# Kernel optimization log

Hardware: AMD Instinct MI355X
Metric: run time of the kernel (lower is better)

The kernel has to match this reference:

```python
import jax, jax.numpy as jnp
import numpy as np
from jax import lax

NUM_MELS = 80
NQ = 256          # num_quants
WIN = 1024
HOP = 256
K_UP = 800        # upsample kernel
PAD_UP = K_UP + 4 * HOP - WIN   # = 800
RC = 120          # residual_channels
SC = 240          # skip_channels
KC = 2            # causal kernel
NB = 16           # num blocks
DILS = [1, 2, 4, 8, 16, 32, 64, 128] * 2
DN = ('NCH', 'OIH', 'NCH')


def conv1x1(x, w, b):
    # x: [B,C,T], w: [O,C], b: [O]
    return jnp.einsum('bct,oc->bot', x, w) + b[None, :, None]


def causal_conv(x, w, b, d):
    # x: [B,RC,T], w: [2RC,RC,KC], left-pad by d*(KC-1) -> causal, same length
    y = lax.conv_general_dilated(x, w, (1,), [(d * (KC - 1), 0)],
                                 rhs_dilation=(d,), dimension_numbers=DN)
    return y + b[None, :, None]


def setup_inputs() -> dict:
    key = jax.random.key(0)
    ks = jax.random.split(key, 20)
    s = 0.05
    n = jax.random.normal
    return {
        'waveforms': n(ks[0], (1, 40960), jnp.float32),
        'melspecs': n(ks[1], (1, NUM_MELS, 160), jnp.float32),
        # ConvTranspose-equivalent upsample weight, stored as direct conv weight [O,I,K]
        'up_w': s * n(ks[2], (NUM_MELS, NUM_MELS, K_UP), jnp.float32),
        'up_b': jnp.zeros((NUM_MELS,), jnp.float32),
        'in_w': s * n(ks[3], (RC, 1), jnp.float32),
        'in_b': jnp.zeros((RC,), jnp.float32),
        'blk_causal_w': s * n(ks[4], (NB, 2 * RC, RC, KC), jnp.float32),
        'blk_causal_b': jnp.zeros((NB, 2 * RC), jnp.float32),
        'blk_cond_w': s * n(ks[5], (NB, 2 * RC, NUM_MELS), jnp.float32),
        'blk_cond_b': jnp.zeros((NB, 2 * RC), jnp.float32),
        'blk_skip_w': s * n(ks[6], (NB, SC, RC), jnp.float32),
        'blk_skip_b': jnp.zeros((NB, SC), jnp.float32),
        'blk_res_w': s * n(ks[7], (NB, RC, RC), jnp.float32),
        'blk_res_b': jnp.zeros((NB, RC), jnp.float32),
        'h1_w': s * n(ks[8], (NQ, SC), jnp.float32),
        'h1_b': jnp.zeros((NQ,), jnp.float32),
        'h2_w': s * n(ks[9], (NQ, NQ), jnp.float32),
        'h2_b': jnp.zeros((NQ,), jnp.float32),
    }


def _forward(waveforms, melspecs, up_w, up_b, in_w, in_b,
             blk_causal_w, blk_causal_b, blk_cond_w, blk_cond_b,
             blk_skip_w, blk_skip_b, blk_res_w, blk_res_b,
             h1_w, h1_b, h2_w, h2_b):
    # ConvTranspose1d(stride=HOP, padding=PAD_UP) as lhs-dilated conv:
    # out_len = (F-1)*HOP + K_UP - 2*PAD_UP
    cond = lax.conv_general_dilated(
        melspecs, up_w, (1,), [(K_UP - 1 - PAD_UP, K_UP - 1 - PAD_UP)],
        lhs_dilation=(HOP,), dimension_numbers=DN) + up_b[None, :, None]
    L = min(waveforms.shape[-1], cond.shape[-1])
    wav = waveforms[..., :L]
    cond = cond[..., :L]

    res = conv1x1(wav[:, None, :], in_w, in_b)          # [B,RC,L]
    skip_sum = jnp.zeros((res.shape[0], SC, L), res.dtype)
    for i, d in enumerate(DILS):
        z = causal_conv(res, blk_causal_w[i], blk_causal_b[i], d) \
            + conv1x1(cond, blk_cond_w[i], blk_cond_b[i])  # [B,2RC,L]
        h = jnp.tanh(z[:, :RC]) * jax.nn.sigmoid(z[:, RC:])
        skip_sum = skip_sum + conv1x1(h, blk_skip_w[i], blk_skip_b[i])
        res = res + conv1x1(h, blk_res_w[i], blk_res_b[i])

    x = jax.nn.relu(skip_sum)
    x = jax.nn.relu(conv1x1(x, h1_w, h1_b))
    logits = conv1x1(x, h2_w, h2_b)                      # [B,NQ,L]
    return logits


def reference(waveforms, melspecs, up_w, up_b, in_w, in_b,
              blk_causal_w, blk_causal_b, blk_cond_w, blk_cond_b,
              blk_skip_w, blk_skip_b, blk_res_w, blk_res_b,
              h1_w, h1_b, h2_w, h2_b):
    return _forward(waveforms, melspecs, up_w, up_b, in_w, in_b,
                    blk_causal_w, blk_causal_b, blk_cond_w, blk_cond_b,
                    blk_skip_w, blk_skip_b, blk_res_w, blk_res_b,
                    h1_w, h1_b, h2_w, h2_b)
```

## Files before the change

kernel.cpp:

```cpp
#include <hip/hip_runtime.h>

#define L_LEN 39904
#define NT 624
#define RCH 120
#define SCH 240
#define CMEL 80
#define NQO 256
#define NBLK 16
#define KUP 800

typedef unsigned short u16;
typedef __attribute__((ext_vector_type(8))) short short8;
typedef __attribute__((ext_vector_type(4))) float f32x4;

#define MFMA(a, b, c) __builtin_amdgcn_mfma_f32_16x16x32_bf16((a), (b), (c), 0, 0, 0)

__device__ __forceinline__ u16 f2bf(float f) {
    unsigned u = __float_as_uint(f);
    u += 0x7FFFu + ((u >> 16) & 1u);
    return (u16)(u >> 16);
}
__device__ __forceinline__ unsigned pack2(float a, float b) {
    return (unsigned)f2bf(a) | ((unsigned)f2bf(b) << 16);
}
__device__ __forceinline__ float b16tof(u16 h) {
    return __uint_as_float((unsigned)h << 16);
}
__device__ __forceinline__ float gate(float a, float b) {
    float ea = __expf(2.f * a);
    float th = 1.f - 2.f * __builtin_amdgcn_rcpf(ea + 1.f);
    float sg = __builtin_amdgcn_rcpf(1.f + __expf(-b));
    return th * sg;
}

constexpr size_t O_CONDT = 0;
constexpr size_t O_RESA  = O_CONDT + 7023104;
constexpr size_t O_RESB  = O_RESA + 19153920;
constexpr size_t O_SKIP  = O_RESB + 19153920;
constexpr size_t O_ZFRAG = O_SKIP + 19153920;
constexpr size_t O_SKF   = O_ZFRAG + 2621440;
constexpr size_t O_RF    = O_SKF + 1048576;
constexpr size_t O_H1F   = O_RF + 524288;
constexpr size_t O_H2F   = O_H1F + 131072;
constexpr size_t O_UPF   = O_H2F + 131072;
constexpr size_t O_ZB    = O_UPF + 13107200;
constexpr size_t O_SKB   = O_ZB + 16384;

constexpr size_t HO_RESA  = 7023104;
constexpr size_t HO_RESB  = HO_RESA + 19153920;
constexpr size_t HO_ZFRAG = HO_RESB + 19153920;
constexpr size_t HO_SKF   = HO_ZFRAG + 2621440;
constexpr size_t HO_RF    = HO_SKF + 1048576;
constexpr size_t HO_H1F   = HO_RF + 524288;
constexpr size_t HO_H2F   = HO_H1F + 131072;
constexpr size_t HO_ZB    = HO_H2F + 131072;
constexpr size_t HO_SKBS  = HO_ZB + 16384;
constexpr size_t HO_HALL  = HO_SKBS + 16384;
constexpr size_t H_BYTES  = (size_t)NBLK * L_LEN * 120 * 2;
constexpr size_t UPF_BYTES = 13107200;
constexpr size_t NEED_H = HO_HALL + (H_BYTES > UPF_BYTES ? H_BYTES : UPF_BYTES);

__global__ void k_prep_zfrag(const float* __restrict__ bc_w, const float* __restrict__ bq_w,
                             u16* __restrict__ dst) {
    int i = blockIdx.x * 256 + threadIdx.x;
    if (i >= NBLK * 10 * 16 * 512) return;
    int jj = i & 7, lane = (i >> 3) & 63, mt = (i >> 9) & 15;
    int rest = i >> 13, ks = rest % 10, blk = rest / 10;
    int m = mt * 16 + (lane & 15);
    int k = ks * 32 + ((lane >> 4) << 3) + jj;
    float v = 0.f;
    if (m < 240) {
        int o = (m & 1) ? (m >> 1) + 120 : (m >> 1);
        if (k < 120)       v = bc_w[((size_t)(blk * 240 + o) * 120 + k) * 2 + 0];
        else if (k < 240)  v = bc_w[((size_t)(blk * 240 + o) * 120 + (k - 120)) * 2 + 1];
        else               v = bq_w[(size_t)(blk * 240 + o) * 80 + (k - 240)];
    }
    dst[i] = f2bf(v);
}
__global__ void k_prep_skfrag(const float* __restrict__ bs_w, u16* __restrict__ dst) {
    int i = blockIdx.x * 256 + threadIdx.x;
    if (i >= NBLK * 4 * 16 * 512) return;
    int jj = i & 7, lane = (i >> 3) & 63, mt = (i >> 9) & 15;
    int rest = i >> 13, ks = rest & 3, blk = rest >> 2;
    int m = mt * 16 + (lane & 15);
    int k = ks * 32 + ((lane >> 4) << 3) + jj;
    float v = (m < 240 && k < 120) ? bs_w[(size_t)(blk * 240 + m) * 120 + k] : 0.f;
    dst[i] = f2bf(v);
}
__global__ void k_prep_rfrag(const float* __restrict__ br_w, u16* __restrict__ dst) {
    int i = blockIdx.x * 256 + threadIdx.x;
    if (i >= NBLK * 4 * 8 * 512) return;
    int jj = i & 7, lane = (i >> 3) & 63, mt = (i >> 9) & 7;
    int rest = i >> 12, ks = rest & 3, blk = rest >> 2;
    int m = mt * 16 + (lane & 15);
    int k = ks * 32 + ((lane >> 4) << 3) + jj;
    float v = (m < 120 && k < 120) ? br_w[(size_t)(blk * 120 + m) * 120 + k] : 0.f;
    dst[i] = f2bf(v);
}
__global__ void k_prep_h1frag(const float* __restrict__ h1_w, u16* __restrict__ dst) {
    int i = blockIdx.x * 256 + threadIdx.x;
    if (i >= 8 * 16 * 512) return;
    int jj = i & 7, lane = (i >> 3) & 63, mt = (i >> 9) & 15, ks = i >> 13;
    int m = mt * 16 + (lane & 15);
    int k = ks * 32 + ((lane >> 4) << 3) + jj;
    float v = (k < 240) ? h1_w[(size_t)m * 240 + k] : 0.f;
    dst[i] = f2bf(v);
}
__global__ void k_prep_h2frag(const float* __restrict__ h2_w, u16* __restrict__ dst) {
    int i = blockIdx.x * 256 + threadIdx.x;
    if (i >= 8 * 16 * 512) return;
    int jj = i & 7, lane = (i >> 3) & 63, mt = (i >> 9) & 15, ks = i >> 13;
    int m = mt * 16 + (lane & 15);
    int k = ks * 32 + ((lane >> 4) << 3) + jj;
    dst[i] = f2bf(h2_w[(size_t)m * 256 + k]);
}
__global__ void k_prep_upfrag(const float* __restrict__ up_w, u16* __restrict__ dst) {
    int i = blockIdx.x * 256 + threadIdx.x;
    if (i >= 256 * 10 * 5 * 512) return;
    int jj = i & 7, lane = (i >> 3) & 63;
    int rest = i >> 9;
    int mt = rest % 5; rest /= 5;
    int ks = rest % 10; int p = rest / 10;
    int m = mt * 16 + (lane & 15);
    int k = ks * 32 + ((lane >> 4) << 3) + jj;
    int c = k >> 2, j = k & 3;
    int r = (256 - ((p + 1) & 255)) & 255;
    int kk = r + 256 * j;
    float v = (m < 80 && kk < KUP) ? up_w[((size_t)m * 80 + c) * KUP + kk] : 0.f;
    dst[i] = f2bf(v);
}
__global__ void k_prep_zbias(const float* __restrict__ bc_b, const float* __restrict__ bq_b,
                             float* __restrict__ dst) {
    int i = blockIdx.x * 256 + threadIdx.x;
    if (i >= NBLK * 256) return;
    int m = i & 255, blk = i >> 8;
    float v = 0.f;
    if (m < 240) {
        int o = (m & 1) ? (m >> 1) + 120 : (m >> 1);
        v = bc_b[blk * 240 + o] + bq_b[blk * 240 + o];
    }
    dst[i] = v;
}
__global__ void k_prep_skbias(const float* __restrict__ bs_b, float* __restrict__ dst) {
    int i = blockIdx.x * 256 + threadIdx.x;
    if (i >= NBLK * 240) return;
    dst[i] = bs_b[i];
}
__global__ void k_prep_skbsum(const float* __restrict__ bs_b, float* __restrict__ dst) {
    int m = blockIdx.x * 256 + threadIdx.x;
    if (m >= 240) return;
    float s = 0.f;
    for (int i = 0; i < NBLK; i++) s += bs_b[i * 240 + m];
    dst[m] = s;
}
__global__ void k_res_initT(const float* __restrict__ wav, const float* __restrict__ in_w,
                            const float* __restrict__ in_b, float* __restrict__ resT) {
    int i = blockIdx.x * 256 + threadIdx.x;
    if (i >= L_LEN * RCH) return;
    int t = i / RCH, c = i % RCH;
    resT[i] = wav[t] * in_w[c] + in_b[c];
}

__global__ __launch_bounds__(256) void k_up(const float* __restrict__ mel,
        const u16* __restrict__ upf, const float* __restrict__ up_b,
        u16* __restrict__ condT) {
    __shared__ u16 s_ms[64 * 328];
    const int tid = threadIdx.x, l = tid & 63, w = tid >> 6;
    const int quad = l >> 4, tloc = l & 15;
    const int p = blockIdx.x, s0 = blockIdx.y * 64;
    for (int rr = 0; rr < 16; rr++) {
        int tt = w + 4 * rr;
        int sg = s0 + tt;
        #pragma unroll
        for (int base = 0; base < 320; base += 64) {
            int ck = base + l;
            int c = ck >> 2, j = ck & 3;
            int mi = 1 + j + sg;
            float v = (mi < 160) ? mel[c * 160 + mi] : 0.f;
            s_ms[tt * 328 + ck] = f2bf(v);
        }
    }
    __syncthreads();
    f32x4 acc[2][4];
    #pragma unroll
    for (int i = 0; i < 2; i++)
        #pragma unroll
        for (int n = 0; n < 4; n++) acc[i][n] = (f32x4){0.f, 0.f, 0.f, 0.f};
    const int nmt = (w == 0) ? 2 : 1;
    int mts[2]; mts[0] = w; mts[1] = 4;
    for (int ks = 0; ks < 10; ks++) {
        short8 b[4];
        int k0 = ks * 32 + quad * 8;
        #pragma unroll
        for (int n = 0; n < 4; n++)
            b[n] = *(const short8*)&s_ms[(n * 16 + tloc) * 328 + k0];
        const short8* ap = (const short8*)(upf) + ((size_t)p * 10 + ks) * 5 * 64;
        for (int i = 0; i < nmt; i++) {
            short8 a = ap[mts[i] * 64 + l];
            #pragma unroll
            for (int n = 0; n < 4; n++) acc[i][n] = MFMA(a, b[n], acc[i][n]);
        }
    }
    for (int i = 0; i < nmt; i++) {
        int o_base = mts[i] * 16 + quad * 4;
        float4 ub = *(const float4*)(up_b + o_base);
        float bb[4] = {ub.x, ub.y, ub.z, ub.w};
        #pragma unroll
        for (int n = 0; n < 4; n++) {
            int sg = s0 + n * 16 + tloc;
            int t = p + 256 * sg;
            if (t < L_LEN) {
                #pragma unroll
                for (int r = 0; r < 4; r++)
                    condT[(size_t)t * 88 + o_base + r] = f2bf(acc[i][n][r] + bb[r]);
            }
        }
    }
}

__global__ __launch_bounds__(512, 4) void k_block(
        const u16* __restrict__ condT, const float* __restrict__ resT_in,
        float* __restrict__ resT_out, u16* __restrict__ skipT,
        const u16* __restrict__ zfrag, const u16* __restrict__ skfrag,
        const u16* __restrict__ rfrag, const float* __restrict__ zbias,
        const float* __restrict__ skbias, const float* __restrict__ resb,
        int blk, int dil, int first) {
    __shared__ u16 s_x[64 * 328];
    u16* s_h = s_x;
    const int tid = threadIdx.x, l = tid & 63, w = tid >> 6;
    const int quad = l >> 4, tloc = l & 15;
    const int t0 = blockIdx.x * 64;
    const short8* zap = (const short8*)(zfrag) + (size_t)blk * 10 * 16 * 64;
    short8 a_cur[2], a_nxt[2];
    #pragma unroll
    for (int i = 0; i < 2; i++) a_cur[i] = zap[(size_t)(w * 2 + i) * 64 + l];
    for (int rr = 0; rr < 8; rr++) {
        int tt = w + 8 * rr;
        int tg = t0 + tt, tp = tg - dil;
        if (l < 60) {
            float2 pv = make_float2(0.f, 0.f), cv = make_float2(0.f, 0.f);
            if (tp >= 0 && tp < L_LEN) pv = *(const float2*)(resT_in + (size_t)tp * 120 + 2 * l);
            if (tg < L_LEN)            cv = *(const float2*)(resT_in + (size_t)tg * 120 + 2 * l);
            *(unsigned*)&s_x[tt * 328 + 2 * l]       = pack2(pv.x, pv.y);
            *(unsigned*)&s_x[tt * 328 + 120 + 2 * l] = pack2(cv.x, cv.y);
        }
        if (l < 40) {
            unsigned q = 0;
            if (tg < L_LEN) q = *(const unsigned*)(condT + (size_t)tg * 88 + 2 * l);
            *(unsigned*)&s_x[tt * 328 + 240 + 2 * l] = q;
        }
    }
    __syncthreads();
    f32x4 acc[2][4];
    #pragma unroll
    for (int i = 0; i < 2; i++)
        #pragma unroll
        for (int n = 0; n < 4; n++) acc[i][n] = (f32x4){0.f, 0.f, 0.f, 0.f};
    for (int ks = 0; ks < 10; ks++) {
        if (ks < 9) {
            #pragma unroll
            for (int i = 0; i < 2; i++)
                a_nxt[i] = zap[((size_t)(ks + 1) * 16 + w * 2 + i) * 64 + l];
        }
        int k0 = ks * 32 + quad * 8;
        short8 b[4];
        #pragma unroll
        for (int n = 0; n < 4; n++)
            b[n] = *(const short8*)&s_x[(n * 16 + tloc) * 328 + k0];
        #pragma unroll
        for (int i = 0; i < 2; i++)
            #pragma unroll
            for (int n = 0; n < 4; n++) acc[i][n] = MFMA(a_cur[i], b[n], acc[i][n]);
        #pragma unroll
        for (int i = 0; i < 2; i++) a_cur[i] = a_nxt[i];
    }
    const short8* sap = (const short8*)(skfrag) + (size_t)blk * 4 * 16 * 64;
    const short8* rap = (const short8*)(rfrag) + (size_t)blk * 4 * 8 * 64;
    short8 sa_c[2], sa_n[2], ra_c, ra_n;
    #pragma unroll
    for (int i = 0; i < 2; i++) sa_c[i] = sap[(size_t)(w * 2 + i) * 64 + l];
    ra_c = rap[(size_t)w * 64 + l];
    uint2 skp[2][4];
    if (!first) {
        #pragma unroll
        for (int i = 0; i < 2; i++) {
            int m_base = (w * 2 + i) * 16 + quad * 4;
            if (m_base < 240) {
                #pragma unroll
                for (int n = 0; n < 4; n++) {
                    int t = t0 + n * 16 + tloc;
                    if (t < L_LEN)
                        skp[i][n] = *(const uint2*)(skipT + (size_t)t * 240 + m_base);
                }
            }
        }
    }
    unsigned hu[2][4];
    #pragma unroll
    for (int i = 0; i < 2; i++) {
        int m_base = (w * 2 + i) * 16 + quad * 4;
        float4 bz4 = *(const float4*)(zbias + blk * 256 + m_base);
        #pragma unroll
        for (int n = 0; n < 4; n++) {
            float h0 = gate(acc[i][n][0] + bz4.x, acc[i][n][1] + bz4.y);
            float h1 = gate(acc[i][n][2] + bz4.z, acc[i][n][3] + bz4.w);
            hu[i][n] = pack2(h0, h1);
        }
    }
    __syncthreads();
    #pragma unroll
    for (int i = 0; i < 2; i++) {
        int j0 = (w * 2 + i) * 8 + quad * 2;
        #pragma unroll
        for (int n = 0; n < 4; n++)
            *(unsigned*)&s_h[(n * 16 + tloc) * 136 + j0] = hu[i][n];
    }
    __syncthreads();
    f32x4 sacc[2][4], racc[4];
    #pragma unroll
    for (int i = 0; i < 2; i++)
        #pragma unroll
        for (int n = 0; n < 4; n++) sacc[i][n] = (f32x4){0.f, 0.f, 0.f, 0.f};
    #pragma unroll
    for (int n = 0; n < 4; n++) racc[n] = (f32x4){0.f, 0.f, 0.f, 0.f};
    for (int ks = 0; ks < 4; ks++) {
        if (ks < 3) {
            #pragma unroll
            for (int i = 0; i < 2; i++)
                sa_n[i] = sap[((size_t)(ks + 1) * 16 + w * 2 + i) * 64 + l];
            ra_n = rap[((size_t)(ks + 1) * 8 + w) * 64 + l];
        }
        short8 b[4];
        int k0 = ks * 32 + quad * 8;
        #pragma unroll
        for (int n = 0; n < 4; n++)
            b[n] = *(const short8*)&s_h[(n * 16 + tloc) * 136 + k0];
        #pragma unroll
        for (int i = 0; i < 2; i++)
            #pragma unroll
            for (int n = 0; n < 4; n++) sacc[i][n] = MFMA(sa_c[i], b[n], sacc[i][n]);
        #pragma unroll
        for (int n = 0; n < 4; n++) racc[n] = MFMA(ra_c, b[n], racc[n]);
        #pragma unroll
        for (int i = 0; i < 2; i++) sa_c[i] = sa_n[i];
        ra_c = ra_n;
    }
    #pragma unroll
    for (int i = 0; i < 2; i++) {
        int m_base = (w * 2 + i) * 16 + quad * 4;
        if (m_base >= 240) continue;
        float4 sb4 = *(const float4*)(skbias + blk * 240 + m_base);
        #pragma unroll
        for (int n = 0; n < 4; n++) {
            int t = t0 + n * 16 + tloc;
            if (t >= L_LEN) continue;
            float x0 = sacc[i][n][0] + sb4.x;
            float x1 = sacc[i][n][1] + sb4.y;
            float x2 = sacc[i][n][2] + sb4.z;
            float x3 = sacc[i][n][3] + sb4.w;
            if (!first) {
                uint2 pv = skp[i][n];
                x0 += b16tof((u16)(pv.x & 0xFFFF));
                x1 += b16tof((u16)(pv.x >> 16));
                x2 += b16tof((u16)(pv.y & 0xFFFF));
                x3 += b16tof((u16)(pv.y >> 16));
            }
            uint2 ov;
            ov.x = pack2(x0, x1);
            ov.y = pack2(x2, x3);
            *(uint2*)(skipT + (size_t)t * 240 + m_base) = ov;
        }
    }
    {
        int m_base = w * 16 + quad * 4;
        if (m_base < 120) {
            float4 rb4 = *(const float4*)(resb + blk * 120 + m_base);
            #pragma unroll
            for (int n = 0; n < 4; n++) {
                int t = t0 + n * 16 + tloc;
                if (t >= L_LEN) continue;
                float4 cur = *(const float4*)(resT_in + (size_t)t * 120 + m_base);
                float4 o;
                o.x = cur.x + racc[n][0] + rb4.x;
                o.y = cur.y + racc[n][1] + rb4.y;
                o.z = cur.z + racc[n][2] + rb4.z;
                o.w = cur.w + racc[n][3] + rb4.w;
                *(float4*)(resT_out + (size_t)t * 120 + m_base) = o;
            }
        }
    }
}

__global__ __launch_bounds__(512, 4) void k_block_h(
        const u16* __restrict__ condT, const float* __restrict__ resT_in,
        float* __restrict__ resT_out, u16* __restrict__ hout,
        const u16* __restrict__ zfrag, const u16* __restrict__ rfrag,
        const float* __restrict__ zbias, const float* __restrict__ resb,
        int blk, int dil) {
    __shared__ u16 s_x[64 * 328];
    u16* s_h = s_x;
    const int tid = threadIdx.x, l = tid & 63, w = tid >> 6;
    const int quad = l >> 4, tloc = l & 15;
    const int t0 = blockIdx.x * 64;
    const short8* zap = (const short8*)(zfrag) + (size_t)blk * 10 * 16 * 64;
    short8 a_cur[2], a_nxt[2];
    a_cur[0] = zap[(size_t)(w * 2 + 0) * 64 + l];
    a_cur[1] = zap[(size_t)(w * 2 + 1) * 64 + l];
    for (int rr = 0; rr < 8; rr++) {
        int tt = w + 8 * rr, tg = t0 + tt;
        if (l < 60) {
            float2 cv = make_float2(0.f, 0.f);
            if (tg < L_LEN) cv = *(const float2*)(resT_in + (size_t)tg * 120 + 2 * l);
            *(unsigned*)&s_x[tt * 328 + 120 + 2 * l] = pack2(cv.x, cv.y);
            if (tt < dil) {
                int tp = tg - dil;
                float2 pv = make_float2(0.f, 0.f);
                if (tp >= 0 && tp < L_LEN) pv = *(const float2*)(resT_in + (size_t)tp * 120 + 2 * l);
                *(unsigned*)&s_x[tt * 328 + 2 * l] = pack2(pv.x, pv.y);
            }
        }
        if (l < 40) {
            unsigned q = 0;
            if (tg < L_LEN) q = *(const unsigned*)(condT + (size_t)tg * 88 + 2 * l);
            *(unsigned*)&s_x[tt * 328 + 240 + 2 * l] = q;
        }
    }
    __syncthreads();
    if (dil < 64) {
        for (int rr = 0; rr < 8; rr++) {
            int tt = w + 8 * rr;
            if (l < 60 && tt >= dil)
                *(unsigned*)&s_x[tt * 328 + 2 * l] =
                    *(const unsigned*)&s_x[(tt - dil) * 328 + 120 + 2 * l];
        }
        __syncthreads();
    }
    f32x4 acc[2][4];
    #pragma unroll
    for (int i = 0; i < 2; i++)
        #pragma unroll
        for (int n = 0; n < 4; n++) acc[i][n] = (f32x4){0.f, 0.f, 0.f, 0.f};
    for (int ks = 0; ks < 10; ks++) {
        if (ks < 9) {
            #pragma unroll
            for (int i = 0; i < 2; i++)
                a_nxt[i] = zap[((size_t)(ks + 1) * 16 + w * 2 + i) * 64 + l];
        }
        int k0 = ks * 32 + quad * 8;
        short8 b[4];
        #pragma unroll
        for (int n = 0; n < 4; n++)
            b[n] = *(const short8*)&s_x[(n * 16 + tloc) * 328 + k0];
        #pragma unroll
        for (int i = 0; i < 2; i++)
            #pragma unroll
            for (int n = 0; n < 4; n++) acc[i][n] = MFMA(a_cur[i], b[n], acc[i][n]);
        #pragma unroll
        for (int i = 0; i < 2; i++) a_cur[i] = a_nxt[i];
    }
    const short8* rap = (const short8*)(rfrag) + (size_t)blk * 4 * 8 * 64;
    short8 ra_c = rap[(size_t)w * 64 + l], ra_n;
    const int m_r = w * 16 + quad * 4;
    float4 cur_pf[4] = {};
    if (m_r < 120) {
        #pragma unroll
        for (int n = 0; n < 4; n++) {
            int t = t0 + n * 16 + tloc;
            if (t < L_LEN) cur_pf[n] = *(const float4*)(resT_in + (size_t)t * 120 + m_r);
        }
    }
    unsigned hu[2][4];
    #pragma unroll
    for (int i = 0; i < 2; i++) {
        int m_base = (w * 2 + i) * 16 + quad * 4;
        float4 bz4 = *(const float4*)(zbias + blk * 256 + m_base);
        #pragma unroll
        for (int n = 0; n < 4; n++) {
            float h0 = gate(acc[i][n][0] + bz4.x, acc[i][n][1] + bz4.y);
            float h1 = gate(acc[i][n][2] + bz4.z, acc[i][n][3] + bz4.w);
            hu[i][n] = pack2(h0, h1);
        }
    }
    __syncthreads();
    #pragma unroll
    for (int i = 0; i < 2; i++) {
        int j0 = (w * 2 + i) * 8 + quad * 2;
        #pragma unroll
        for (int n = 0; n < 4; n++)
            *(unsigned*)&s_h[(n * 16 + tloc) * 136 + j0] = hu[i][n];
    }
    __syncthreads();
    for (int rr = 0; rr < 8; rr++) {
        int tt = w + 8 * rr, tg = t0 + tt;
        if (l < 60 && tg < L_LEN)
            *(unsigned*)&hout[(size_t)tg * 120 + 2 * l] =
                *(const unsigned*)&s_h[tt * 136 + 2 * l];
    }
    f32x4 racc[4];
    #pragma unroll
    for (int n = 0; n < 4; n++) racc[n] = (f32x4){0.f, 0.f, 0.f, 0.f};
    for (int ks = 0; ks < 4; ks++) {
        if (ks < 3) ra_n = rap[((size_t)(ks + 1) * 8 + w) * 64 + l];
        short8 b[4];
        int k0 = ks * 32 + quad * 8;
        #pragma unroll
        for (int n = 0; n < 4; n++)
            b[n] = *(const short8*)&s_h[(n * 16 + tloc) * 136 + k0];
        #pragma unroll
        for (int n = 0; n < 4; n++) racc[n] = MFMA(ra_c, b[n], racc[n]);
        ra_c = ra_n;
    }
    if (m_r < 120) {
        float4 rb4 = *(const float4*)(resb + blk * 120 + m_r);
        #pragma unroll
        for (int n = 0; n < 4; n++) {
            int t = t0 + n * 16 + tloc;
            if (t >= L_LEN) continue;
            float4 o;
            o.x = cur_pf[n].x + racc[n][0] + rb4.x;
            o.y = cur_pf[n].y + racc[n][1] + rb4.y;
            o.z = cur_pf[n].z + racc[n][2] + rb4.z;
            o.w = cur_pf[n].w + racc[n][3] + rb4.w;
            *(float4*)(resT_out + (size_t)t * 120 + m_r) = o;
        }
    }
}

__global__ __launch_bounds__(512, 4) void k_final(const u16* __restrict__ skipT,
        const u16* __restrict__ h1f, const u16* __restrict__ h2f,
        const float* __restrict__ h1_b, const float* __restrict__ h2_b,
        float* __restrict__ out) {
    __shared__ u16 s_m[64 * 264];
    const int tid = threadIdx.x, l = tid & 63, w = tid >> 6;
    const int quad = l >> 4, tloc = l & 15;
    const int t0 = blockIdx.x * 64;
    const short8* ap1 = (const short8*)h1f;
    short8 a_cur[2], a_nxt[2];
    #pragma unroll
    for (int i = 0; i < 2; i++) a_cur[i] = ap1[(size_t)(w * 2 + i) * 64 + l];
    for (int rr = 0; rr < 8; rr++) {
        int tt = w + 8 * rr;
        int tg = t0 + tt;
        uint2 v = make_uint2(0u, 0u);
        if (l < 60 && tg < L_LEN)
            v = *(const uint2*)(skipT + (size_t)tg * 240 + 4 * l);
        float x0 = fmaxf(b16tof((u16)(v.x & 0xFFFF)), 0.f);
        float x1 = fmaxf(b16tof((u16)(v.x >> 16)), 0.f);
        float x2 = fmaxf(b16tof((u16)(v.y & 0xFFFF)), 0.f);
        float x3 = fmaxf(b16tof((u16)(v.y >> 16)), 0.f);
        uint2 ov;
        ov.x = pack2(x0, x1);
        ov.y = pack2(x2, x3);
        *(uint2*)&s_m[tt * 264 + 4 * l] = ov;
    }
    __syncthreads();
    f32x4 acc[2][4];
    #pragma unroll
    for (int i = 0; i < 2; i++)
        #pragma unroll
        for (int n = 0; n < 4; n++) acc[i][n] = (f32x4){0.f, 0.f, 0.f, 0.f};
    for (int ks = 0; ks < 8; ks++) {
        if (ks < 7) {
            #pragma unroll
            for (int i = 0; i < 2; i++)
                a_nxt[i] = ap1[((size_t)(ks + 1) * 16 + w * 2 + i) * 64 + l];
        }
        short8 b[4];
        int k0 = ks * 32 + quad * 8;
        #pragma unroll
        for (int n = 0; n < 4; n++)
            b[n] = *(const short8*)&s_m[(n * 16 + tloc) * 264 + k0];
        #pragma unroll
        for (int i = 0; i < 2; i++)
            #pragma unroll
            for (int n = 0; n < 4; n++) acc[i][n] = MFMA(a_cur[i], b[n], acc[i][n]);
        #pragma unroll
        for (int i = 0; i < 2; i++) a_cur[i] = a_nxt[i];
    }
    unsigned ylo[2][4], yhi[2][4];
    #pragma unroll
    for (int i = 0; i < 2; i++) {
        int m_base = (w * 2 + i) * 16 + quad * 4;
        float4 b1 = *(const float4*)(h1_b + m_base);
        #pragma unroll
        for (int n = 0; n < 4; n++) {
            float y0 = fmaxf(acc[i][n][0] + b1.x, 0.f);
            float y1v = fmaxf(acc[i][n][1] + b1.y, 0.f);
            float y2 = fmaxf(acc[i][n][2] + b1.z, 0.f);
            float y3 = fmaxf(acc[i][n][3] + b1.w, 0.f);
            ylo[i][n] = pack2(y0, y1v);
            yhi[i][n] = pack2(y2, y3);
        }
    }
    const short8* ap2 = (const short8*)h2f;
    #pragma unroll
    for (int i = 0; i < 2; i++) a_cur[i] = ap2[(size_t)(w * 2 + i) * 64 + l];
    __syncthreads();
    #pragma unroll
    for (int i = 0; i < 2; i++) {
        int m_base = (w * 2 + i) * 16 + quad * 4;
        #pragma unroll
        for (int n = 0; n < 4; n++) {
            int t = n * 16 + tloc;
            *(unsigned*)&s_m[t * 264 + m_base]     = ylo[i][n];
            *(unsigned*)&s_m[t * 264 + m_base + 2] = yhi[i][n];
        }
    }
    __syncthreads();
    #pragma unroll
    for (int i = 0; i < 2; i++)
        #pragma unroll
        for (int n = 0; n < 4; n++) acc[i][n] = (f32x4){0.f, 0.f, 0.f, 0.f};
    for (int ks = 0; ks < 8; ks++) {
        if (ks < 7) {
            #pragma unroll
            for (int i = 0; i < 2; i++)
                a_nxt[i] = ap2[((size_t)(ks + 1) * 16 + w * 2 + i) * 64 + l];
        }
        short8 b[4];
        int k0 = ks * 32 + quad * 8;
        #pragma unroll
        for (int n = 0; n < 4; n++)
            b[n] = *(const short8*)&s_m[(n * 16 + tloc) * 264 + k0];
        #pragma unroll
        for (int i = 0; i < 2; i++)
            #pragma unroll
            for (int n = 0; n < 4; n++) acc[i][n] = MFMA(a_cur[i], b[n], acc[i][n]);
        #pragma unroll
        for (int i = 0; i < 2; i++) a_cur[i] = a_nxt[i];
    }
    #pragma unroll
    for (int i = 0; i < 2; i++) {
        int m_base = (w * 2 + i) * 16 + quad * 4;
        float4 b2 = *(const float4*)(h2_b + m_base);
        float bb[4] = {b2.x, b2.y, b2.z, b2.w};
        #pragma unroll
        for (int n = 0; n < 4; n++) {
            int t = t0 + n * 16 + tloc;
            if (t >= L_LEN) continue;
            #pragma unroll
            for (int r = 0; r < 4; r++)
                out[(size_t)(m_base + r) * L_LEN + t] = acc[i][n][r] + bb[r];
        }
    }
}

__global__ __launch_bounds__(512, 4) void k_final_h(const u16* __restrict__ hall,
        const u16* __restrict__ skf, const u16* __restrict__ h1f,
        const u16* __restrict__ h2f, const float* __restrict__ skbsum,
        const float* __restrict__ h1_b, const float* __restrict__ h2_b,
        float* __restrict__ out) {
    __shared__ u16 s_m[64 * 264];
    const int tid = threadIdx.x, l = tid & 63, w = tid >> 6;
    const int quad = l >> 4, tloc = l & 15;
    const int t0 = blockIdx.x * 64;
    const short8* sap = (const short8*)skf;

    unsigned ha[8], hb[8];
    auto LOADH = [&](unsigned (&reg)[8], int i) {
        const u16* hp = hall + (size_t)i * ((size_t)L_LEN * 120);
        #pragma unroll
        for (int rr = 0; rr < 8; rr++) {
            int tg = t0 + w + 8 * rr;
            reg[rr] = (l < 60 && tg < L_LEN)
                ? *(const unsigned*)&hp[(size_t)tg * 120 + 2 * l] : 0u;
        }
    };
    LOADH(ha, 0);
    short8 sa_c[2], sa_n[2];
    sa_c[0] = sap[(size_t)(w * 2 + 0) * 64 + l];
    sa_c[1] = sap[(size_t)(w * 2 + 1) * 64 + l];
    f32x4 sacc[2][4];
    #pragma unroll
    for (int i = 0; i < 2; i++)
        #pragma unroll
        for (int n = 0; n < 4; n++) sacc[i][n] = (f32x4){0.f, 0.f, 0.f, 0.f};

    auto SKSTEP = [&](unsigned (&cur)[8], unsigned (&nxt)[8], int i, bool donext) {
        __syncthreads();
        #pragma unroll
        for (int rr = 0; rr < 8; rr++) {
            int off = (w + 8 * rr) * 264 + 2 * l;
            if (l < 60)          *(unsigned*)&s_m[off] = cur[rr];
            else if (i == 0)     *(unsigned*)&s_m[off] = 0u;
        }
        __syncthreads();
        if (donext) LOADH(nxt, i + 1);
        for (int ks = 0; ks < 4; ks++) {
            int g = i * 4 + ks;
            if (g < 63) {
                sa_n[0] = sap[((size_t)(g + 1) * 16 + w * 2 + 0) * 64 + l];
                sa_n[1] = sap[((size_t)(g + 1) * 16 + w * 2 + 1) * 64 + l];
            }
            int k0 = ks * 32 + quad * 8;
            short8 b[4];
            #pragma unroll
            for (int n = 0; n < 4; n++)
                b[n] = *(const short8*)&s_m[(n * 16 + tloc) * 264 + k0];
            #pragma unroll
            for (int i2 = 0; i2 < 2; i2++)
                #pragma unroll
                for (int n = 0; n < 4; n++)
                    sacc[i2][n] = MFMA(sa_c[i2], b[n], sacc[i2][n]);
            sa_c[0] = sa_n[0]; sa_c[1] = sa_n[1];
        }
    };
    for (int ii = 0; ii < 16; ii += 2) {
        SKSTEP(ha, hb, ii, true);
        SKSTEP(hb, ha, ii + 1, ii + 1 < 15);
    }
    __syncthreads();
    const short8* ap1 = (const short8*)h1f;
    short8 a_cur[2], a_nxt[2];
    a_cur[0] = ap1[(size_t)(w * 2 + 0) * 64 + l];
    a_cur[1] = ap1[(size_t)(w * 2 + 1) * 64 + l];
    #pragma unroll
    for (int i2 = 0; i2 < 2; i2++) {
        int m_base = (w * 2 + i2) * 16 + quad * 4;
        float4 sb4 = make_float4(0.f, 0.f, 0.f, 0.f);
        bool valid = (m_base < 240);
        if (valid) sb4 = *(const float4*)(skbsum + m_base);
        #pragma unroll
        for (int n = 0; n < 4; n++) {
            float x0 = 0.f, x1 = 0.f, x2 = 0.f, x3 = 0.f;
            if (valid) {
                x0 = fmaxf(sacc[i2][n][0] + sb4.x, 0.f);
                x1 = fmaxf(sacc[i2][n][1] + sb4.y, 0.f);
                x2 = fmaxf(sacc[i2][n][2] + sb4.z, 0.f);
                x3 = fmaxf(sacc[i2][n][3] + sb4.w, 0.f);
            }
            int t = n * 16 + tloc;
            *(unsigned*)&s_m[t * 264 + m_base]     = pack2(x0, x1);
            *(unsigned*)&s_m[t * 264 + m_base + 2] = pack2(x2, x3);
        }
    }
    __syncthreads();
    f32x4 acc[2][4];
    #pragma unroll
    for (int i = 0; i < 2; i++)
        #pragma unroll
        for (int n = 0; n < 4; n++) acc[i][n] = (f32x4){0.f, 0.f, 0.f, 0.f};
    for (int ks = 0; ks < 8; ks++) {
        if (ks < 7) {
            #pragma unroll
            for (int i = 0; i < 2; i++)
                a_nxt[i] = ap1[((size_t)(ks + 1) * 16 + w * 2 + i) * 64 + l];
        }
        short8 b[4];
        int k0 = ks * 32 + quad * 8;
        #pragma unroll
        for (int n = 0; n < 4; n++)
            b[n] = *(const short8*)&s_m[(n * 16 + tloc) * 264 + k0];
        #pragma unroll
        for (int i = 0; i < 2; i++)
            #pragma unroll
            for (int n = 0; n < 4; n++) acc[i][n] = MFMA(a_cur[i], b[n], acc[i][n]);
        #pragma unroll
        for (int i = 0; i < 2; i++) a_cur[i] = a_nxt[i];
    }
    unsigned ylo[2][4], yhi[2][4];
    #pragma unroll
    for (int i = 0; i < 2; i++) {
        int m_base = (w * 2 + i) * 16 + quad * 4;
        float4 b1 = *(const float4*)(h1_b + m_base);
        #pragma unroll
        for (int n = 0; n < 4; n++) {
            float y0 = fmaxf(acc[i][n][0] + b1.x, 0.f);
            float y1v = fmaxf(acc[i][n][1] + b1.y, 0.f);
            float y2 = fmaxf(acc[i][n][2] + b1.z, 0.f);
            float y3 = fmaxf(acc[i][n][3] + b1.w, 0.f);
            ylo[i][n] = pack2(y0, y1v);
            yhi[i][n] = pack2(y2, y3);
        }
    }
    const short8* ap2 = (const short8*)h2f;
    #pragma unroll
    for (int i = 0; i < 2; i++) a_cur[i] = ap2[(size_t)(w * 2 + i) * 64 + l];
    __syncthreads();
    #pragma unroll
    for (int i = 0; i < 2; i++) {
        int m_base = (w * 2 + i) * 16 + quad * 4;
        #pragma unroll
        for (int n = 0; n < 4; n++) {
            int t = n * 16 + tloc;
            *(unsigned*)&s_m[t * 264 + m_base]     = ylo[i][n];
            *(unsigned*)&s_m[t * 264 + m_base + 2] = yhi[i][n];
        }
    }
    __syncthreads();
    #pragma unroll
    for (int i = 0; i < 2; i++)
        #pragma unroll
        for (int n = 0; n < 4; n++) acc[i][n] = (f32x4){0.f, 0.f, 0.f, 0.f};
    for (int ks = 0; ks < 8; ks++) {
        if (ks < 7) {
            #pragma unroll
            for (int i = 0; i < 2; i++)
                a_nxt[i] = ap2[((size_t)(ks + 1) * 16 + w * 2 + i) * 64 + l];
        }
        short8 b[4];
        int k0 = ks * 32 + quad * 8;
        #pragma unroll
        for (int n = 0; n < 4; n++)
            b[n] = *(const short8*)&s_m[(n * 16 + tloc) * 264 + k0];
        #pragma unroll
        for (int i = 0; i < 2; i++)
            #pragma unroll
            for (int n = 0; n < 4; n++) acc[i][n] = MFMA(a_cur[i], b[n], acc[i][n]);
        #pragma unroll
        for (int i = 0; i < 2; i++) a_cur[i] = a_nxt[i];
    }
    #pragma unroll
    for (int i = 0; i < 2; i++) {
        int m_base = (w * 2 + i) * 16 + quad * 4;
        float4 b2 = *(const float4*)(h2_b + m_base);
        float bb[4] = {b2.x, b2.y, b2.z, b2.w};
        #pragma unroll
        for (int n = 0; n < 4; n++) {
            int t = t0 + n * 16 + tloc;
            if (t >= L_LEN) continue;
            #pragma unroll
            for (int r = 0; r < 4; r++)
                out[(size_t)(m_base + r) * L_LEN + t] = acc[i][n][r] + bb[r];
        }
    }
}

extern "C" void kernel_launch(void* const* d_in, const int* in_sizes, int n_in,
                              void* d_out, int out_size, void* d_ws, size_t ws_size,
                              hipStream_t stream) {
    const float* wav   = (const float*)d_in[0];
    const float* mel   = (const float*)d_in[1];
    const float* up_w  = (const float*)d_in[2];
    const float* up_b  = (const float*)d_in[3];
    const float* in_w  = (const float*)d_in[4];
    const float* in_b  = (const float*)d_in[5];
    const float* bc_w  = (const float*)d_in[6];
    const float* bc_b  = (const float*)d_in[7];
    const float* bq_w  = (const float*)d_in[8];
    const float* bq_b  = (const float*)d_in[9];
    const float* bs_w  = (const float*)d_in[10];
    const float* bs_b  = (const float*)d_in[11];
    const float* br_w  = (const float*)d_in[12];
    const float* br_b  = (const float*)d_in[13];
    const float* h1_w  = (const float*)d_in[14];
    const float* h1_b  = (const float*)d_in[15];
    const float* h2_w  = (const float*)d_in[16];
    const float* h2_b  = (const float*)d_in[17];

    char* wsb = (char*)d_ws;
    const bool use_h = (ws_size >= NEED_H);

    if (use_h) {
        u16*   condT = (u16*)(wsb + 0);
        float* resA  = (float*)(wsb + HO_RESA);
        float* resB  = (float*)(wsb + HO_RESB);
        u16*   zfrag = (u16*)(wsb + HO_ZFRAG);
        u16*   skf   = (u16*)(wsb + HO_SKF);
        u16*   rf    = (u16*)(wsb + HO_RF);
        u16*   h1f   = (u16*)(wsb + HO_H1F);
        u16*   h2f   = (u16*)(wsb + HO_H2F);
        float* zb    = (float*)(wsb + HO_ZB);
        float* skbs  = (float*)(wsb + HO_SKBS);
        u16*   hall  = (u16*)(wsb + HO_HALL);
        u16*   upf   = (u16*)(wsb + HO_HALL);

        k_prep_zfrag <<<5120, 256, 0, stream>>>(bc_w, bq_w, zfrag);
        k_prep_skfrag<<<2048, 256, 0, stream>>>(bs_w, skf);
        k_prep_rfrag <<<1024, 256, 0, stream>>>(br_w, rf);
        k_prep_h1frag<<<256, 256, 0, stream>>>(h1_w, h1f);
        k_prep_h2frag<<<256, 256, 0, stream>>>(h2_w, h2f);
        k_prep_upfrag<<<25600, 256, 0, stream>>>(up_w, upf);
        k_prep_zbias <<<16, 256, 0, stream>>>(bc_b, bq_b, zb);
        k_prep_skbsum<<<1, 256, 0, stream>>>(bs_b, skbs);
        k_res_initT  <<<(L_LEN * RCH + 255) / 256, 256, 0, stream>>>(wav, in_w, in_b, resA);
        k_up<<<dim3(256, 3), 256, 0, stream>>>(mel, upf, up_b, condT);

        for (int i = 0; i < NBLK; i++) {
            int d = 1 << (i & 7);
            const float* rin = (i & 1) ? resB : resA;
            float* rout      = (i & 1) ? resA : resB;
            k_block_h<<<NT, 512, 0, stream>>>(condT, rin, rout,
                                              hall + (size_t)i * (size_t)L_LEN * 120,
                                              zfrag, rf, zb, br_b, i, d);
        }
        k_final_h<<<NT, 512, 0, stream>>>(hall, skf, h1f, h2f, skbs, h1_b, h2_b,
                                          (float*)d_out);
    } else {
        u16*   condT = (u16*)(wsb + O_CONDT);
        float* resA  = (float*)(wsb + O_RESA);
        float* resB  = (float*)(wsb + O_RESB);
        u16*   skipT = (u16*)(wsb + O_SKIP);
        u16*   zfrag = (u16*)(wsb + O_ZFRAG);
        u16*   skf   = (u16*)(wsb + O_SKF);
        u16*   rf    = (u16*)(wsb + O_RF);
        u16*   h1f   = (u16*)(wsb + O_H1F);
        u16*   h2f   = (u16*)(wsb + O_H2F);
        u16*   upf   = (u16*)(wsb + O_UPF);
        float* zb    = (float*)(wsb + O_ZB);
        float* skb   = (float*)(wsb + O_SKB);

        k_prep_zfrag <<<5120, 256, 0, stream>>>(bc_w, bq_w, zfrag);
        k_prep_skfrag<<<2048, 256, 0, stream>>>(bs_w, skf);
        k_prep_rfrag <<<1024, 256, 0, stream>>>(br_w, rf);
        k_prep_h1frag<<<256, 256, 0, stream>>>(h1_w, h1f);
        k_prep_h2frag<<<256, 256, 0, stream>>>(h2_w, h2f);
        k_prep_upfrag<<<25600, 256, 0, stream>>>(up_w, upf);
        k_prep_zbias <<<16, 256, 0, stream>>>(bc_b, bq_b, zb);
        k_prep_skbias<<<15, 256, 0, stream>>>(bs_b, skb);
        k_res_initT  <<<(L_LEN * RCH + 255) / 256, 256, 0, stream>>>(wav, in_w, in_b, resA);
        k_up<<<dim3(256, 3), 256, 0, stream>>>(mel, upf, up_b, condT);

        for (int i = 0; i < NBLK; i++) {
            int d = 1 << (i & 7);
            const float* rin = (i & 1) ? resB : resA;
            float* rout      = (i & 1) ? resA : resB;
            k_block<<<NT, 512, 0, stream>>>(condT, rin, rout, skipT, zfrag, skf, rf,
                                            zb, skb, br_b, i, d, (i == 0) ? 1 : 0);
        }
        k_final<<<NT, 512, 0, stream>>>(skipT, h1f, h2f, h1_b, h2_b, (float*)d_out);
    }
}
```

Baseline: 757.2 us.

## Keep bf16 residual copy and load MFMA B fragments directly from global

The residual stream is now kept as an fp32 master buffer updated in place, plus a ping-pong bf16 copy written by each block. The gated conv and final skip kernels read their MFMA B operands straight from global memory into registers, with register double-buffering, instead of staging tiles through shared memory with barriers. This removes the LDS staging, the shifted-copy pass for dilation and several __syncthreads. In exchange it relies on cache hits for the overlapping time rows, adds a bf16 store per block, and issues more scattered 16-byte global loads.

```diff
diff --git a/kernel.cpp b/kernel.cpp
--- a/kernel.cpp
+++ b/kernel.cpp
@@ -46,19 +46,21 @@
 constexpr size_t O_ZB    = O_UPF + 13107200;
 constexpr size_t O_SKB   = O_ZB + 16384;
 
-constexpr size_t HO_RESA  = 7023104;
-constexpr size_t HO_RESB  = HO_RESA + 19153920;
-constexpr size_t HO_ZFRAG = HO_RESB + 19153920;
-constexpr size_t HO_SKF   = HO_ZFRAG + 2621440;
-constexpr size_t HO_RF    = HO_SKF + 1048576;
-constexpr size_t HO_H1F   = HO_RF + 524288;
-constexpr size_t HO_H2F   = HO_H1F + 131072;
-constexpr size_t HO_ZB    = HO_H2F + 131072;
-constexpr size_t HO_SKBS  = HO_ZB + 16384;
-constexpr size_t HO_HALL  = HO_SKBS + 16384;
+constexpr size_t H2_CONDT = 0;
+constexpr size_t H2_RESF  = 7023104;
+constexpr size_t H2_BFA   = H2_RESF + 19153920;
+constexpr size_t H2_BFB   = H2_BFA + 9576960;
+constexpr size_t H2_ZFRAG = H2_BFB + 9576960;
+constexpr size_t H2_SKF   = H2_ZFRAG + 2621440;
+constexpr size_t H2_RF    = H2_SKF + 1048576;
+constexpr size_t H2_H1F   = H2_RF + 524288;
+constexpr size_t H2_H2F   = H2_H1F + 131072;
+constexpr size_t H2_ZB    = H2_H2F + 131072;
+constexpr size_t H2_SKBS  = H2_ZB + 16384;
+constexpr size_t H2_HALL  = H2_SKBS + 16384;
 constexpr size_t H_BYTES  = (size_t)NBLK * L_LEN * 120 * 2;
 constexpr size_t UPF_BYTES = 13107200;
-constexpr size_t NEED_H = HO_HALL + (H_BYTES > UPF_BYTES ? H_BYTES : UPF_BYTES);
+constexpr size_t NEED_H = H2_HALL + (H_BYTES > UPF_BYTES ? H_BYTES : UPF_BYTES);
 
 __global__ void k_prep_zfrag(const float* __restrict__ bc_w, const float* __restrict__ bq_w,
                              u16* __restrict__ dst) {
@@ -159,6 +161,16 @@
     if (i >= L_LEN * RCH) return;
     int t = i / RCH, c = i % RCH;
     resT[i] = wav[t] * in_w[c] + in_b[c];
+}
+__global__ void k_res_initT2(const float* __restrict__ wav, const float* __restrict__ in_w,
+                             const float* __restrict__ in_b, float* __restrict__ resT,
+                             u16* __restrict__ resB) {
+    int i = blockIdx.x * 256 + threadIdx.x;
+    if (i >= L_LEN * RCH) return;
+    int t = i / RCH, c = i % RCH;
+    float v = wav[t] * in_w[c] + in_b[c];
+    resT[i] = v;
+    resB[i] = f2bf(v);
 }
 
 __global__ __launch_bounds__(256) void k_up(const float* __restrict__ mel,
@@ -391,72 +403,77 @@
     }
 }
 
-__global__ __launch_bounds__(512, 4) void k_block_h(
-        const u16* __restrict__ condT, const float* __restrict__ resT_in,
-        float* __restrict__ resT_out, u16* __restrict__ hout,
+__global__ __launch_bounds__(512, 4) void k_block_h2(
+        const u16* __restrict__ condT, float* __restrict__ resF,
+        const u16* __restrict__ bfIn, u16* __restrict__ bfOut,
+        u16* __restrict__ hout,
         const u16* __restrict__ zfrag, const u16* __restrict__ rfrag,
         const float* __restrict__ zbias, const float* __restrict__ resb,
         int blk, int dil) {
-    __shared__ u16 s_x[64 * 328];
-    u16* s_h = s_x;
+    __shared__ u16 s_h[64 * 136];
     const int tid = threadIdx.x, l = tid & 63, w = tid >> 6;
     const int quad = l >> 4, tloc = l & 15;
     const int t0 = blockIdx.x * 64;
+    const short8 ZV = {0, 0, 0, 0, 0, 0, 0, 0};
+    int oP[4], oC[4], oQ[4];
+    bool pz[4];
+    #pragma unroll
+    for (int n = 0; n < 4; n++) {
+        int tn = t0 + n * 16 + tloc;
+        int tc = tn < L_LEN ? tn : L_LEN - 1;
+        int tp = tn - dil;
+        pz[n] = (tp < 0);
+        int tpc = tp < 0 ? 0 : (tp < L_LEN ? tp : L_LEN - 1);
+        oP[n] = tpc * 120;
+        oC[n] = tc * 120;
+        oQ[n] = tc * 88;
+    }
     const short8* zap = (const short8*)(zfrag) + (size_t)blk * 10 * 16 * 64;
     short8 a_cur[2], a_nxt[2];
     a_cur[0] = zap[(size_t)(w * 2 + 0) * 64 + l];
     a_cur[1] = zap[(size_t)(w * 2 + 1) * 64 + l];
-    for (int rr = 0; rr < 8; rr++) {
-        int tt = w + 8 * rr, tg = t0 + tt;
-        if (l < 60) {
-            float2 cv = make_float2(0.f, 0.f);
-            if (tg < L_LEN) cv = *(const float2*)(resT_in + (size_t)tg * 120 + 2 * l);
-            *(unsigned*)&s_x[tt * 328 + 120 + 2 * l] = pack2(cv.x, cv.y);
-            if (tt < dil) {
-                int tp = tg - dil;
-                float2 pv = make_float2(0.f, 0.f);
-                if (tp >= 0 && tp < L_LEN) pv = *(const float2*)(resT_in + (size_t)tp * 120 + 2 * l);
-                *(unsigned*)&s_x[tt * 328 + 2 * l] = pack2(pv.x, pv.y);
-            }
-        }
-        if (l < 40) {
-            unsigned q = 0;
-            if (tg < L_LEN) q = *(const unsigned*)(condT + (size_t)tg * 88 + 2 * l);
-            *(unsigned*)&s_x[tt * 328 + 240 + 2 * l] = q;
-        }
-    }
-    __syncthreads();
-    if (dil < 64) {
-        for (int rr = 0; rr < 8; rr++) {
-            int tt = w + 8 * rr;
-            if (l < 60 && tt >= dil)
-                *(unsigned*)&s_x[tt * 328 + 2 * l] =
-                    *(const unsigned*)&s_x[(tt - dil) * 328 + 120 + 2 * l];
-        }
-        __syncthreads();
-    }
     f32x4 acc[2][4];
     #pragma unroll
     for (int i = 0; i < 2; i++)
         #pragma unroll
         for (int n = 0; n < 4; n++) acc[i][n] = (f32x4){0.f, 0.f, 0.f, 0.f};
+    short8 bc[4], bn[4];
+    {
+        int k0 = quad * 8;
+        #pragma unroll
+        for (int n = 0; n < 4; n++) {
+            short8 v = *(const short8*)(bfIn + oP[n] + k0);
+            if (pz[n]) v = ZV;
+            bc[n] = v;
+        }
+    }
+    #pragma unroll
     for (int ks = 0; ks < 10; ks++) {
         if (ks < 9) {
-            #pragma unroll
-            for (int i = 0; i < 2; i++)
-                a_nxt[i] = zap[((size_t)(ks + 1) * 16 + w * 2 + i) * 64 + l];
-        }
-        int k0 = ks * 32 + quad * 8;
-        short8 b[4];
-        #pragma unroll
-        for (int n = 0; n < 4; n++)
-            b[n] = *(const short8*)&s_x[(n * 16 + tloc) * 328 + k0];
+            int k1 = (ks + 1) * 32 + quad * 8;
+            #pragma unroll
+            for (int n = 0; n < 4; n++) {
+                short8 v;
+                if (k1 < 120) {
+                    v = *(const short8*)(bfIn + oP[n] + k1);
+                    if (pz[n]) v = ZV;
+                } else if (k1 < 240) {
+                    v = *(const short8*)(bfIn + oC[n] + (k1 - 120));
+                } else {
+                    v = *(const short8*)(condT + oQ[n] + (k1 - 240));
+                }
+                bn[n] = v;
+            }
+            a_nxt[0] = zap[((size_t)(ks + 1) * 16 + w * 2 + 0) * 64 + l];
+            a_nxt[1] = zap[((size_t)(ks + 1) * 16 + w * 2 + 1) * 64 + l];
+        }
         #pragma unroll
         for (int i = 0; i < 2; i++)
             #pragma unroll
-            for (int n = 0; n < 4; n++) acc[i][n] = MFMA(a_cur[i], b[n], acc[i][n]);
-        #pragma unroll
-        for (int i = 0; i < 2; i++) a_cur[i] = a_nxt[i];
+            for (int n = 0; n < 4; n++) acc[i][n] = MFMA(a_cur[i], bc[n], acc[i][n]);
+        #pragma unroll
+        for (int n = 0; n < 4; n++) bc[n] = bn[n];
+        a_cur[0] = a_nxt[0]; a_cur[1] = a_nxt[1];
     }
     const short8* rap = (const short8*)(rfrag) + (size_t)blk * 4 * 8 * 64;
     short8 ra_c = rap[(size_t)w * 64 + l], ra_n;
@@ -466,7 +483,7 @@
         #pragma unroll
         for (int n = 0; n < 4; n++) {
             int t = t0 + n * 16 + tloc;
-            if (t < L_LEN) cur_pf[n] = *(const float4*)(resT_in + (size_t)t * 120 + m_r);
+            if (t < L_LEN) cur_pf[n] = *(const float4*)(resF + (size_t)t * 120 + m_r);
         }
     }
     unsigned hu[2][4];
@@ -481,7 +498,6 @@
             hu[i][n] = pack2(h0, h1);
         }
     }
-    __syncthreads();
     #pragma unroll
     for (int i = 0; i < 2; i++) {
         int j0 = (w * 2 + i) * 8 + quad * 2;
@@ -521,7 +537,11 @@
             o.y = cur_pf[n].y + racc[n][1] + rb4.y;
             o.z = cur_pf[n].z + racc[n][2] + rb4.z;
             o.w = cur_pf[n].w + racc[n][3] + rb4.w;
-            *(float4*)(resT_out + (size_t)t * 120 + m_r) = o;
+            *(float4*)(resF + (size_t)t * 120 + m_r) = o;
+            uint2 hv;
+            hv.x = pack2(o.x, o.y);
+            hv.y = pack2(o.z, o.w);
+            *(uint2*)(bfOut + (size_t)t * 120 + m_r) = hv;
         }
     }
 }
@@ -645,7 +665,7 @@
     }
 }
 
-__global__ __launch_bounds__(512, 4) void k_final_h(const u16* __restrict__ hall,
+__global__ __launch_bounds__(512, 4) void k_final_h2(const u16* __restrict__ hall,
         const u16* __restrict__ skf, const u16* __restrict__ h1f,
         const u16* __restrict__ h2f, const float* __restrict__ skbsum,
         const float* __restrict__ h1_b, const float* __restrict__ h2_b,
@@ -654,19 +674,16 @@
     const int tid = threadIdx.x, l = tid & 63, w = tid >> 6;
     const int quad = l >> 4, tloc = l & 15;
     const int t0 = blockIdx.x * 64;
+    const short8 ZV = {0, 0, 0, 0, 0, 0, 0, 0};
+    int ro[4];
+    #pragma unroll
+    for (int n = 0; n < 4; n++) {
+        int tn = t0 + n * 16 + tloc;
+        ro[n] = (tn < L_LEN ? tn : L_LEN - 1) * 120;
+    }
+    const bool kpad = (quad == 3);
+    const int k0q = quad * 8;
     const short8* sap = (const short8*)skf;
-
-    unsigned ha[8], hb[8];
-    auto LOADH = [&](unsigned (&reg)[8], int i) {
-        const u16* hp = hall + (size_t)i * ((size_t)L_LEN * 120);
-        #pragma unroll
-        for (int rr = 0; rr < 8; rr++) {
-            int tg = t0 + w + 8 * rr;
-            reg[rr] = (l < 60 && tg < L_LEN)
-                ? *(const unsigned*)&hp[(size_t)tg * 120 + 2 * l] : 0u;
-        }
-    };
-    LOADH(ha, 0);
     short8 sa_c[2], sa_n[2];
     sa_c[0] = sap[(size_t)(w * 2 + 0) * 64 + l];
     sa_c[1] = sap[(size_t)(w * 2 + 1) * 64 + l];
@@ -675,41 +692,34 @@
     for (int i = 0; i < 2; i++)
         #pragma unroll
         for (int n = 0; n < 4; n++) sacc[i][n] = (f32x4){0.f, 0.f, 0.f, 0.f};
-
-    auto SKSTEP = [&](unsigned (&cur)[8], unsigned (&nxt)[8], int i, bool donext) {
-        __syncthreads();
-        #pragma unroll
-        for (int rr = 0; rr < 8; rr++) {
-            int off = (w + 8 * rr) * 264 + 2 * l;
-            if (l < 60)          *(unsigned*)&s_m[off] = cur[rr];
-            else if (i == 0)     *(unsigned*)&s_m[off] = 0u;
-        }
-        __syncthreads();
-        if (donext) LOADH(nxt, i + 1);
-        for (int ks = 0; ks < 4; ks++) {
-            int g = i * 4 + ks;
-            if (g < 63) {
-                sa_n[0] = sap[((size_t)(g + 1) * 16 + w * 2 + 0) * 64 + l];
-                sa_n[1] = sap[((size_t)(g + 1) * 16 + w * 2 + 1) * 64 + l];
+    short8 bc[4], bn[4];
+    #pragma unroll
+    for (int n = 0; n < 4; n++)
+        bc[n] = *(const short8*)(hall + ro[n] + k0q);
+    for (int g = 0; g < 64; g++) {
+        if (g < 63) {
+            int g1 = g + 1;
+            const u16* hp = hall + (size_t)(g1 >> 2) * ((size_t)L_LEN * 120);
+            int kk = (g1 & 3) * 32 + k0q;
+            bool pad = ((g1 & 3) == 3) && kpad;
+            #pragma unroll
+            for (int n = 0; n < 4; n++) {
+                short8 v = *(const short8*)(hp + ro[n] + kk);
+                if (pad) v = ZV;
+                bn[n] = v;
             }
-            int k0 = ks * 32 + quad * 8;
-            short8 b[4];
+            sa_n[0] = sap[((size_t)g1 * 16 + w * 2 + 0) * 64 + l];
+            sa_n[1] = sap[((size_t)g1 * 16 + w * 2 + 1) * 64 + l];
+        }
+        #pragma unroll
+        for (int i2 = 0; i2 < 2; i2++)
             #pragma unroll
             for (int n = 0; n < 4; n++)
-                b[n] = *(const short8*)&s_m[(n * 16 + tloc) * 264 + k0];
-            #pragma unroll
-            for (int i2 = 0; i2 < 2; i2++)
-                #pragma unroll
-                for (int n = 0; n < 4; n++)
-                    sacc[i2][n] = MFMA(sa_c[i2], b[n], sacc[i2][n]);
-            sa_c[0] = sa_n[0]; sa_c[1] = sa_n[1];
-        }
-    };
-    for (int ii = 0; ii < 16; ii += 2) {
-        SKSTEP(ha, hb, ii, true);
-        SKSTEP(hb, ha, ii + 1, ii + 1 < 15);
-    }
-    __syncthreads();
+                sacc[i2][n] = MFMA(sa_c[i2], bc[n], sacc[i2][n]);
+        #pragma unroll
+        for (int n = 0; n < 4; n++) bc[n] = bn[n];
+        sa_c[0] = sa_n[0]; sa_c[1] = sa_n[1];
+    }
     const short8* ap1 = (const short8*)h1f;
     short8 a_cur[2], a_nxt[2];
     a_cur[0] = ap1[(size_t)(w * 2 + 0) * 64 + l];
@@ -852,18 +862,19 @@
     const bool use_h = (ws_size >= NEED_H);
 
     if (use_h) {
-        u16*   condT = (u16*)(wsb + 0);
-        float* resA  = (float*)(wsb + HO_RESA);
-        float* resB  = (float*)(wsb + HO_RESB);
-        u16*   zfrag = (u16*)(wsb + HO_ZFRAG);
-        u16*   skf   = (u16*)(wsb + HO_SKF);
-        u16*   rf    = (u16*)(wsb + HO_RF);
-        u16*   h1f   = (u16*)(wsb + HO_H1F);
-        u16*   h2f   = (u16*)(wsb + HO_H2F);
-        float* zb    = (float*)(wsb + HO_ZB);
-        float* skbs  = (float*)(wsb + HO_SKBS);
-        u16*   hall  = (u16*)(wsb + HO_HALL);
-        u16*   upf   = (u16*)(wsb + HO_HALL);
+        u16*   condT = (u16*)(wsb + H2_CONDT);
+        float* resF  = (float*)(wsb + H2_RESF);
+        u16*   bfA   = (u16*)(wsb + H2_BFA);
+        u16*   bfB   = (u16*)(wsb + H2_BFB);
+        u16*   zfrag = (u16*)(wsb + H2_ZFRAG);
+        u16*   skf   = (u16*)(wsb + H2_SKF);
+        u16*   rf    = (u16*)(wsb + H2_RF);
+        u16*   h1f   = (u16*)(wsb + H2_H1F);
+        u16*   h2f   = (u16*)(wsb + H2_H2F);
+        float* zb    = (float*)(wsb + H2_ZB);
+        float* skbs  = (float*)(wsb + H2_SKBS);
+        u16*   hall  = (u16*)(wsb + H2_HALL);
+        u16*   upf   = (u16*)(wsb + H2_HALL);
 
         k_prep_zfrag <<<5120, 256, 0, stream>>>(bc_w, bq_w, zfrag);
         k_prep_skfrag<<<2048, 256, 0, stream>>>(bs_w, skf);
@@ -873,19 +884,19 @@
         k_prep_upfrag<<<25600, 256, 0, stream>>>(up_w, upf);
         k_prep_zbias <<<16, 256, 0, stream>>>(bc_b, bq_b, zb);
         k_prep_skbsum<<<1, 256, 0, stream>>>(bs_b, skbs);
-        k_res_initT  <<<(L_LEN * RCH + 255) / 256, 256, 0, stream>>>(wav, in_w, in_b, resA);
+        k_res_initT2 <<<(L_LEN * RCH + 255) / 256, 256, 0, stream>>>(wav, in_w, in_b, resF, bfA);
         k_up<<<dim3(256, 3), 256, 0, stream>>>(mel, upf, up_b, condT);
 
         for (int i = 0; i < NBLK; i++) {
             int d = 1 << (i & 7);
-            const float* rin = (i & 1) ? resB : resA;
-            float* rout      = (i & 1) ? resA : resB;
-            k_block_h<<<NT, 512, 0, stream>>>(condT, rin, rout,
-                                              hall + (size_t)i * (size_t)L_LEN * 120,
-                                              zfrag, rf, zb, br_b, i, d);
-        }
-        k_final_h<<<NT, 512, 0, stream>>>(hall, skf, h1f, h2f, skbs, h1_b, h2_b,
-                                          (float*)d_out);
+            const u16* bfIn = (i & 1) ? bfB : bfA;
+            u16* bfOut      = (i & 1) ? bfA : bfB;
+            k_block_h2<<<NT, 512, 0, stream>>>(condT, resF, bfIn, bfOut,
+                                               hall + (size_t)i * (size_t)L_LEN * 120,
+                                               zfrag, rf, zb, br_b, i, d);
+        }
+        k_final_h2<<<NT, 512, 0, stream>>>(hall, skf, h1f, h2f, skbs, h1_b, h2_b,
+                                           (float*)d_out);
     } else {
         u16*   condT = (u16*)(wsb + O_CONDT);
         float* resA  = (float*)(wsb + O_RESA);
```

Result: slower. 804.7 us (+6.3%).
